# Optimization experiments

Hardware: AMD Instinct MI355X
Metric: run time of the kernel (lower is better)

## Reference

```python
import jax, jax.numpy as jnp
import numpy as np

D = 1024
H = 16
HD = D // H
B = 2
T = 2048


def setup_inputs() -> dict:
    key = jax.random.key(0)
    ks = jax.random.split(key, 5)
    x = jax.random.normal(ks[0], (B, T, D), dtype=jnp.float32)
    # PyTorch SDPA bool-mask semantics: True = attend. Causal lower-triangular.
    attn_mask = jnp.tril(jnp.ones((T, T), dtype=bool))
    w_qkv = jax.random.normal(ks[1], (3 * D, D), dtype=jnp.float32) * (1.0 / np.sqrt(D))
    b_qkv = jax.random.normal(ks[2], (3 * D,), dtype=jnp.float32) * 0.02
    w_proj = jax.random.normal(ks[3], (D, D), dtype=jnp.float32) * (1.0 / np.sqrt(D))
    b_proj = jax.random.normal(ks[4], (D,), dtype=jnp.float32) * 0.02
    return {"x": x, "attn_mask": attn_mask, "w_qkv": w_qkv, "b_qkv": b_qkv,
            "w_proj": w_proj, "b_proj": b_proj}


def reference(x, attn_mask, w_qkv, b_qkv, w_proj, b_proj):
    b, t, d = x.shape
    # fused QKV projection (torch Linear: y = x @ W.T + b)
    qkv = jnp.einsum('btd,ed->bte', x, w_qkv) + b_qkv  # [B,T,3D]
    q, k, v = jnp.split(qkv, 3, axis=-1)
    # [B,T,D] -> [B,H,T,hd]
    def heads(z):
        return z.reshape(b, t, H, HD).transpose(0, 2, 1, 3)
    q, k, v = heads(q), heads(k), heads(v)
    scale = 1.0 / jnp.sqrt(jnp.asarray(HD, dtype=x.dtype))
    scores = jnp.einsum('bhqd,bhkd->bhqk', q, k) * scale  # [B,H,T,T]
    neg_inf = jnp.asarray(jnp.finfo(x.dtype).min, dtype=x.dtype)
    scores = jnp.where(attn_mask, scores, neg_inf)
    attn = jax.nn.softmax(scores, axis=-1)
    y = jnp.einsum('bhqk,bhkd->bhqd', attn, v)  # [B,H,T,hd]
    y = y.transpose(0, 2, 1, 3).reshape(b, t, d)
    y = jnp.einsum('btd,ed->bte', y, w_proj) + b_proj
    return y
```

## Files before the change

kernel.cpp:

```cpp
#include <hip/hip_runtime.h>
#include <hip/hip_bf16.h>
#include <math.h>

#define D_MODEL 1024
#define NHEAD   16
#define HDIM    64
#define BATCH   2
#define SEQ     2048
#define MTOT    (BATCH * SEQ)

typedef unsigned short u16;
typedef unsigned int u32;
typedef short short8 __attribute__((ext_vector_type(8)));
typedef float floatx4 __attribute__((ext_vector_type(4)));

#define LOG2E 1.44269504088896340736f

#if __has_builtin(__builtin_amdgcn_exp2f)
#define EXP2(x) __builtin_amdgcn_exp2f(x)
#else
#define EXP2(x) exp2f(x)
#endif

static __device__ __forceinline__ u16 f2b(float f) {
  union { __hip_bfloat16 h; u16 u; } cv;
  cv.h = __float2bfloat16(f);
  return cv.u;
}

typedef const __attribute__((address_space(1))) unsigned int guint;
typedef __attribute__((address_space(3))) unsigned int luint;
static __device__ __forceinline__ void gl_lds16(const u16* g, u16* l) {
  __builtin_amdgcn_global_load_lds((guint*)g, (luint*)l, 16, 0, 0);
}

__global__ __launch_bounds__(256) void cast3_f2b(
    const float* __restrict__ a, u16* __restrict__ ao, int na,
    const float* __restrict__ b, u16* __restrict__ bo, int nb,
    const float* __restrict__ c, u16* __restrict__ co) {
  int i = (blockIdx.x * 256 + threadIdx.x) * 4;
  const float* src;
  u16* dst;
  if (i < na) {
    src = a + i;
    dst = ao + i;
  } else if (i < na + nb) {
    src = b + (i - na);
    dst = bo + (i - na);
  } else {
    src = c + (i - na - nb);
    dst = co + (i - na - nb);
  }
  float4 v = *(const float4*)src;
  ushort4 o;
  o.x = f2b(v.x);
  o.y = f2b(v.y);
  o.z = f2b(v.z);
  o.w = f2b(v.w);
  *(ushort4*)dst = o;
}

template <int MODE, int AR>
__global__ __launch_bounds__(256) void gemm_bt_bf16(
    const u16* __restrict__ A, const u16* __restrict__ Bm,
    const float* __restrict__ bias, u16* __restrict__ Cq, u16* __restrict__ Ck,
    u16* __restrict__ Cvt, float* __restrict__ Cf, int M, int N, int K) {
  constexpr int MI = AR / 32;
  constexpr int SMREQ = 2 * (AR + 128) * 32;
  constexpr int SM = (MODE == 0) ? (SMREQ > 17408 ? SMREQ : 17408) : SMREQ;
  __shared__ u16 smem[SM];
  u16(*As)[AR][32] = (u16(*)[AR][32])smem;
  u16(*Bs)[128][32] = (u16(*)[128][32])(smem + 2 * AR * 32);

  const int tid = threadIdx.x;
  const int lane = tid & 63;
  const int wave = tid >> 6;
  const int wm = (wave >> 1) * (AR / 2);
  const int wn = (wave & 1) * 64;
  const int quad = lane >> 4;
  const int l15 = lane & 15;
  const int m0 = blockIdx.y * AR;
  const int n0 = blockIdx.x * 128;

  const int srow = wave * 16 + (lane >> 2);
  const int k8 = (lane & 3) * 8;

  const u16* gA0 = A + (size_t)(m0 + srow) * K + k8;
  const u16* gA1 = A + (size_t)(m0 + srow + 64) * K + k8;
  const u16* gB0 = Bm + (size_t)(n0 + srow) * K + k8;
  const u16* gB1 = Bm + (size_t)(n0 + srow + 64) * K + k8;

  floatx4 acc[MI][4];
#pragma unroll
  for (int i = 0; i < MI; ++i)
#pragma unroll
    for (int j = 0; j < 4; ++j)
#pragma unroll
      for (int e = 0; e < 4; ++e) acc[i][j][e] = 0.0f;

  gl_lds16(gA0, &As[0][srow][k8]);
  if (AR == 128) gl_lds16(gA1, &As[0][srow + 64][k8]);
  gl_lds16(gB0, &Bs[0][srow][k8]);
  gl_lds16(gB1, &Bs[0][srow + 64][k8]);

  const int niter = K / 32;
  for (int kt = 0; kt < niter; ++kt) {
    const int cur = kt & 1;
    __syncthreads();
    if (kt + 1 < niter) {
      const int k0n = (kt + 1) * 32;
      gl_lds16(gA0 + k0n, &As[cur ^ 1][srow][k8]);
      if (AR == 128) gl_lds16(gA1 + k0n, &As[cur ^ 1][srow + 64][k8]);
      gl_lds16(gB0 + k0n, &Bs[cur ^ 1][srow][k8]);
      gl_lds16(gB1 + k0n, &Bs[cur ^ 1][srow + 64][k8]);
    }
    short8 af[MI], bf[4];
#pragma unroll
    for (int i = 0; i < MI; ++i)
      af[i] = *(const short8*)&As[cur][wm + i * 16 + l15][quad * 8];
#pragma unroll
    for (int j = 0; j < 4; ++j)
      bf[j] = *(const short8*)&Bs[cur][wn + j * 16 + l15][quad * 8];
#pragma unroll
    for (int i = 0; i < MI; ++i)
#pragma unroll
      for (int j = 0; j < 4; ++j)
        acc[i][j] = __builtin_amdgcn_mfma_f32_16x16x32_bf16(af[i], bf[j],
                                                            acc[i][j], 0, 0, 0);
  }

  if (MODE == 0) {
    const int nbase = n0 + wn;
    const int sel = nbase >> 10;
    const int h = (nbase >> 6) & (NHEAD - 1);
    if (sel == 2) {
#pragma unroll
      for (int j = 0; j < 4; ++j) {
        const int n = nbase + j * 16 + l15;
        const float bv = bias[n];
        const int d = n & (HDIM - 1);
#pragma unroll
        for (int i = 0; i < MI; ++i) {
          const int mb = m0 + wm + i * 16 + quad * 4;
          const int b = mb >> 11;
          const int t = mb & (SEQ - 1);
          ushort4 o4;
          o4.x = f2b(acc[i][j][0] + bv);
          o4.y = f2b(acc[i][j][1] + bv);
          o4.z = f2b(acc[i][j][2] + bv);
          o4.w = f2b(acc[i][j][3] + bv);
          *(ushort4*)(Cvt + ((size_t)(b * NHEAD + h) * HDIM + d) * SEQ + t) = o4;
        }
      }
    } else {
      u16* dst = (sel == 0) ? Cq : Ck;
      __syncthreads();
      u16(*Ct)[68] = (u16(*)[68])(smem + wave * 4352);
#pragma unroll
      for (int j = 0; j < 4; ++j) {
        const float bv = bias[nbase + j * 16 + l15];
#pragma unroll
        for (int i = 0; i < MI; ++i)
#pragma unroll
          for (int r = 0; r < 4; ++r)
            Ct[i * 16 + quad * 4 + r][j * 16 + l15] = f2b(acc[i][j][r] + bv);
      }
      const int mb0 = m0 + wm;
      const int b = mb0 >> 11;
      const int t0 = mb0 & (SEQ - 1);
      u16* rowbase = dst + ((size_t)(b * NHEAD + h) * SEQ + t0) * HDIM;
      const int tr = lane >> 3;
      const int d8 = (lane & 7) * 8;
#pragma unroll
      for (int p = 0; p < 8; ++p) {
        const int row = p * 8 + tr;
        *(short8*)(rowbase + (size_t)row * HDIM + d8) =
            *(const short8*)&Ct[row][d8];
      }
    }
  } else {
#pragma unroll
    for (int j = 0; j < 4; ++j) {
      const int n = n0 + wn + j * 16 + l15;
      const float bv = bias[n];
#pragma unroll
      for (int i = 0; i < MI; ++i) {
        const int mb = m0 + wm + i * 16 + quad * 4;
#pragma unroll
        for (int r = 0; r < 4; ++r)
          Cf[(size_t)(mb + r) * N + n] = acc[i][j][r] + bv;
      }
    }
  }
}

__global__ __launch_bounds__(256) void flash_mfma(const u16* __restrict__ Qg,
                                                  const u16* __restrict__ Kg,
                                                  const u16* __restrict__ Vtg,
                                                  u16* __restrict__ Yb) {
  __shared__ u16 Ks[2][64][76];
  __shared__ u16 Vt[2][80][76];
  __shared__ u16 Pb[64][76];

  const int tid = threadIdx.x;
  const int lane = tid & 63;
  const int wave = tid >> 6;
  const int wrow = wave * 16;
  const int quad = lane >> 4;
  const int l15 = lane & 15;
  const int bh = blockIdx.y;
  const int b = bh >> 4;
  const int h = bh & (NHEAD - 1);

  const u16* Qp = Qg + (size_t)bh * SEQ * HDIM;
  const u16* Kp = Kg + (size_t)bh * SEQ * HDIM;
  const u16* Vp = Vtg + (size_t)bh * HDIM * SEQ;

  const int srow = tid >> 2;
  const int sc = (tid & 3) * 16;

  const float scale2 = 0.125f * LOG2E;

#pragma unroll
  for (int bufi = 0; bufi < 2; ++bufi)
    for (int idx = tid; idx < 16 * 38; idx += 256) {
      const int row = 64 + idx / 38;
      const int c2 = (idx % 38) * 2;
      *(u32*)&Vt[bufi][row][c2] = (row == 64 && c2 < 64) ? 0x3F803F80u : 0u;
    }

#pragma unroll
  for (int phase = 0; phase < 2; ++phase) {
    const int qt = phase == 0 ? (16 + blockIdx.x) : (15 - blockIdx.x);
    const int q0 = qt * 64;

    __syncthreads();

    short8 aq[2];
    {
      const u16* qrow = Qp + (size_t)(q0 + wrow + l15) * HDIM + quad * 8;
      aq[0] = *(const short8*)qrow;
      aq[1] = *(const short8*)(qrow + 32);
    }

    floatx4 o[5];
#pragma unroll
    for (int c = 0; c < 5; ++c)
#pragma unroll
      for (int e = 0; e < 4; ++e) o[c][e] = 0.0f;

    const int nkt = qt + 1;
    short8 kv0 = *(const short8*)(Kp + (size_t)srow * HDIM + sc);
    short8 kv1 = *(const short8*)(Kp + (size_t)srow * HDIM + sc + 8);
    short8 vv0 = *(const short8*)(Vp + (size_t)srow * SEQ + sc);
    short8 vv1 = *(const short8*)(Vp + (size_t)srow * SEQ + sc + 8);

    for (int kt = 0; kt < nkt; ++kt) {
      const int k0 = kt * 64;
      const int buf = kt & 1;
      *(short8*)&Ks[buf][srow][sc] = kv0;
      *(short8*)&Ks[buf][srow][sc + 8] = kv1;
      *(short8*)&Vt[buf][srow][sc] = vv0;
      *(short8*)&Vt[buf][srow][sc + 8] = vv1;
      __syncthreads();
      if (kt + 1 < nkt) {
        const u16* kp = Kp + (size_t)(k0 + 64 + srow) * HDIM + sc;
        const u16* vp = Vp + (size_t)srow * SEQ + k0 + 64 + sc;
        kv0 = *(const short8*)kp;
        kv1 = *(const short8*)(kp + 8);
        vv0 = *(const short8*)vp;
        vv1 = *(const short8*)(vp + 8);
      }

      short8 bk[4][2];
#pragma unroll
      for (int c = 0; c < 4; ++c)
#pragma unroll
        for (int kk = 0; kk < 2; ++kk)
          bk[c][kk] =
              *(const short8*)&Ks[buf][c * 16 + l15][kk * 32 + quad * 8];

      floatx4 s[4];
#pragma unroll
      for (int c = 0; c < 4; ++c) {
#pragma unroll
        for (int e = 0; e < 4; ++e) s[c][e] = 0.0f;
        s[c] = __builtin_amdgcn_mfma_f32_16x16x32_bf16(aq[0], bk[c][0], s[c],
                                                       0, 0, 0);
        s[c] = __builtin_amdgcn_mfma_f32_16x16x32_bf16(aq[1], bk[c][1], s[c],
                                                       0, 0, 0);
      }

      const bool msk = (kt == nkt - 1);
      const int prow = wrow + quad * 4;
#pragma unroll
      for (int c = 0; c < 4; ++c)
#pragma unroll
        for (int r = 0; r < 4; ++r) {
          float v = s[c][r] * scale2;
          if (msk) {
            const int row = q0 + prow + r;
            const int col = k0 + c * 16 + l15;
            if (col > row) v = -INFINITY;
          }
          Pb[prow + r][c * 16 + l15] = f2b(EXP2(v));
        }

      short8 ap[2];
#pragma unroll
      for (int kk = 0; kk < 2; ++kk)
        ap[kk] = *(const short8*)&Pb[wrow + l15][kk * 32 + quad * 8];
#pragma unroll
      for (int c = 0; c < 5; ++c) {
        short8 bv0 = *(const short8*)&Vt[buf][c * 16 + l15][quad * 8];
        short8 bv1 = *(const short8*)&Vt[buf][c * 16 + l15][32 + quad * 8];
        o[c] = __builtin_amdgcn_mfma_f32_16x16x32_bf16(ap[0], bv0, o[c], 0, 0,
                                                       0);
        o[c] = __builtin_amdgcn_mfma_f32_16x16x32_bf16(ap[1], bv1, o[c], 0, 0,
                                                       0);
      }
    }

#pragma unroll
    for (int r = 0; r < 4; ++r) {
      const float lr = __shfl(o[4][r], lane & 48);
      const float inv = 1.0f / lr;
      const int t = q0 + wrow + quad * 4 + r;
#pragma unroll
      for (int c = 0; c < 4; ++c)
        Yb[((size_t)b * SEQ + t) * D_MODEL + h * HDIM + c * 16 + l15] =
            f2b(o[c][r] * inv);
    }
  }
}

extern "C" void kernel_launch(void* const* d_in, const int* in_sizes, int n_in,
                              void* d_out, int out_size, void* d_ws,
                              size_t ws_size, hipStream_t stream) {
  const float* x = (const float*)d_in[0];
  const float* w_qkv = (const float*)d_in[2];
  const float* b_qkv = (const float*)d_in[3];
  const float* w_proj = (const float*)d_in[4];
  const float* b_proj = (const float*)d_in[5];
  float* out = (float*)d_out;

  const size_t nx = (size_t)MTOT * D_MODEL;
  const size_t nwq = (size_t)3 * D_MODEL * D_MODEL;
  const size_t nwp = (size_t)D_MODEL * D_MODEL;
  const size_t nqkv = (size_t)BATCH * NHEAD * SEQ * HDIM;

  u16* xb = (u16*)d_ws;
  u16* wqb = xb + nx;
  u16* wpb = wqb + nwq;
  u16* qb = wpb + nwp;
  u16* kb = qb + nqkv;
  u16* vtb = kb + nqkv;
  u16* yb = vtb + nqkv;

  cast3_f2b<<<dim3((nx + nwq + nwp) / 1024), dim3(256), 0, stream>>>(
      x, xb, (int)nx, w_qkv, wqb, (int)nwq, w_proj, wpb);

  gemm_bt_bf16<0, 128><<<dim3(24, 32), dim3(256), 0, stream>>>(
      xb, wqb, b_qkv, qb, kb, vtb, nullptr, MTOT, 3 * D_MODEL, D_MODEL);
  flash_mfma<<<dim3(16, BATCH * NHEAD), dim3(256), 0, stream>>>(qb, kb, vtb,
                                                                yb);
  gemm_bt_bf16<1, 64><<<dim3(8, 64), dim3(256), 0, stream>>>(
      yb, wpb, b_proj, nullptr, nullptr, nullptr, out, MTOT, D_MODEL, D_MODEL);
}
```

Measured before the change: 188.7 us.

## Split flash attention KV tiles across wave pairs and keep P in registers

Restructures the flash attention kernel so that two wave pairs each process alternate 64-key tiles of a two-tile super-step. Each wave owns 32 query rows and computes S transposed so the P fragments can feed a 16x16x16 MFMA directly from registers, which removes the LDS round-trip for P. The row sum is now accumulated explicitly instead of through the extra ones-row V column, and the partial outputs of the two wave pairs are merged through an LDS scratch buffer at the end. This adds an extra barrier per step, wasted work on the odd final tile, and a reduction epilogue.

```diff
diff --git a/kernel.cpp b/kernel.cpp
--- a/kernel.cpp
+++ b/kernel.cpp
@@ -12,6 +12,7 @@
 typedef unsigned short u16;
 typedef unsigned int u32;
 typedef short short8 __attribute__((ext_vector_type(8)));
+typedef short short4v __attribute__((ext_vector_type(4)));
 typedef float floatx4 __attribute__((ext_vector_type(4)));
 
 #define LOG2E 1.44269504088896340736f
@@ -26,6 +27,18 @@
   union { __hip_bfloat16 h; u16 u; } cv;
   cv.h = __float2bfloat16(f);
   return cv.u;
+}
+
+static __device__ __forceinline__ floatx4 mfma16(short4v a, short4v b,
+                                                 floatx4 c) {
+#if __has_builtin(__builtin_amdgcn_mfma_f32_16x16x16bf16_1k)
+  return __builtin_amdgcn_mfma_f32_16x16x16bf16_1k(a, b, c, 0, 0, 0);
+#else
+  asm volatile("v_mfma_f32_16x16x16_bf16 %0, %1, %2, %0"
+               : "+v"(c)
+               : "v"(a), "v"(b));
+  return c;
+#endif
 }
 
 typedef const __attribute__((address_space(1))) unsigned int guint;
@@ -198,14 +211,15 @@
                                                   const u16* __restrict__ Kg,
                                                   const u16* __restrict__ Vtg,
                                                   u16* __restrict__ Yb) {
-  __shared__ u16 Ks[2][64][76];
-  __shared__ u16 Vt[2][80][76];
-  __shared__ u16 Pb[64][76];
+  __shared__ u16 Ks[2][64][72];
+  __shared__ u16 Vt[2][64][72];
+  __shared__ float scr[2][64][36];
 
   const int tid = threadIdx.x;
   const int lane = tid & 63;
   const int wave = tid >> 6;
-  const int wrow = wave * 16;
+  const int par = wave >> 1;
+  const int rhalf = (wave & 1) * 32;
   const int quad = lane >> 4;
   const int l15 = lane & 15;
   const int bh = blockIdx.y;
@@ -217,119 +231,175 @@
   const u16* Vp = Vtg + (size_t)bh * HDIM * SEQ;
 
   const int srow = tid >> 2;
-  const int sc = (tid & 3) * 16;
+  const int scq = (tid & 3) * 16;
 
   const float scale2 = 0.125f * LOG2E;
-
-#pragma unroll
-  for (int bufi = 0; bufi < 2; ++bufi)
-    for (int idx = tid; idx < 16 * 38; idx += 256) {
-      const int row = 64 + idx / 38;
-      const int c2 = (idx % 38) * 2;
-      *(u32*)&Vt[bufi][row][c2] = (row == 64 && c2 < 64) ? 0x3F803F80u : 0u;
-    }
 
 #pragma unroll
   for (int phase = 0; phase < 2; ++phase) {
     const int qt = phase == 0 ? (16 + blockIdx.x) : (15 - blockIdx.x);
     const int q0 = qt * 64;
-
+    const int nkt = qt + 1;
+    const int nsup = (nkt + 1) >> 1;
+
+    short8 aq[2][2];
+#pragma unroll
+    for (int m = 0; m < 2; ++m) {
+      const u16* qrow =
+          Qp + (size_t)(q0 + rhalf + m * 16 + l15) * HDIM + quad * 8;
+      aq[m][0] = *(const short8*)qrow;
+      aq[m][1] = *(const short8*)(qrow + 32);
+    }
+
+    floatx4 o[2][4];
+#pragma unroll
+    for (int m = 0; m < 2; ++m)
+#pragma unroll
+      for (int cd = 0; cd < 4; ++cd)
+#pragma unroll
+        for (int e = 0; e < 4; ++e) o[m][cd][e] = 0.0f;
+    float l_acc[2] = {0.0f, 0.0f};
+
+    short8 rk[2][2], rv[2][2];
+    {
+#pragma unroll
+      for (int t = 0; t < 2; ++t) {
+        const int kb = (t < nkt ? t : nkt - 1) * 64;
+        const u16* kp = Kp + (size_t)(kb + srow) * HDIM + scq;
+        const u16* vp = Vp + (size_t)srow * SEQ + kb + scq;
+        rk[t][0] = *(const short8*)kp;
+        rk[t][1] = *(const short8*)(kp + 8);
+        rv[t][0] = *(const short8*)vp;
+        rv[t][1] = *(const short8*)(vp + 8);
+      }
+    }
+
+    for (int s2 = 0; s2 < nsup; ++s2) {
+#pragma unroll
+      for (int t = 0; t < 2; ++t) {
+        *(short8*)&Ks[t][srow][scq] = rk[t][0];
+        *(short8*)&Ks[t][srow][scq + 8] = rk[t][1];
+        *(short8*)&Vt[t][srow][scq] = rv[t][0];
+        *(short8*)&Vt[t][srow][scq + 8] = rv[t][1];
+      }
+      __syncthreads();
+      if (s2 + 1 < nsup) {
+#pragma unroll
+        for (int t = 0; t < 2; ++t) {
+          const int kt = 2 * s2 + 2 + t;
+          const int kb = (kt < nkt ? kt : nkt - 1) * 64;
+          const u16* kp = Kp + (size_t)(kb + srow) * HDIM + scq;
+          const u16* vp = Vp + (size_t)srow * SEQ + kb + scq;
+          rk[t][0] = *(const short8*)kp;
+          rk[t][1] = *(const short8*)(kp + 8);
+          rv[t][0] = *(const short8*)vp;
+          rv[t][1] = *(const short8*)(vp + 8);
+        }
+      }
+
+      const int my_kt = 2 * s2 + par;
+      if (my_kt < nkt) {
+        const int k0p = my_kt * 64;
+
+        floatx4 st[4][2];
+#pragma unroll
+        for (int ck = 0; ck < 4; ++ck) {
+          const u16* krow = &Ks[par][ck * 16 + l15][quad * 8];
+          const short8 bk0 = *(const short8*)krow;
+          const short8 bk1 = *(const short8*)(krow + 32);
+#pragma unroll
+          for (int m = 0; m < 2; ++m) {
+            floatx4 acc;
+#pragma unroll
+            for (int e = 0; e < 4; ++e) acc[e] = 0.0f;
+            acc = __builtin_amdgcn_mfma_f32_16x16x32_bf16(bk0, aq[m][0], acc,
+                                                          0, 0, 0);
+            acc = __builtin_amdgcn_mfma_f32_16x16x32_bf16(bk1, aq[m][1], acc,
+                                                          0, 0, 0);
+            st[ck][m] = acc;
+          }
+        }
+
+        const bool msk = (my_kt == qt);
+        short4v pl[4][2];
+#pragma unroll
+        for (int ck = 0; ck < 4; ++ck)
+#pragma unroll
+          for (int m = 0; m < 2; ++m) {
+            const int qrow = q0 + rhalf + m * 16 + l15;
+            const int kbase = k0p + ck * 16 + quad * 4;
+            float psum = 0.0f;
+            short4v pv;
+#pragma unroll
+            for (int r = 0; r < 4; ++r) {
+              float p = EXP2(st[ck][m][r] * scale2);
+              if (msk && (kbase + r > qrow)) p = 0.0f;
+              psum += p;
+              pv[r] = (short)f2b(p);
+            }
+            l_acc[m] += psum;
+            pl[ck][m] = pv;
+          }
+
+#pragma unroll
+        for (int ck = 0; ck < 4; ++ck) {
+          short4v bv[4];
+#pragma unroll
+          for (int cd = 0; cd < 4; ++cd)
+            bv[cd] =
+                *(const short4v*)&Vt[par][cd * 16 + l15][ck * 16 + quad * 4];
+#pragma unroll
+          for (int m = 0; m < 2; ++m)
+#pragma unroll
+            for (int cd = 0; cd < 4; ++cd)
+              o[m][cd] = mfma16(pl[ck][m], bv[cd], o[m][cd]);
+        }
+      }
+      __syncthreads();
+    }
+
+#pragma unroll
+    for (int m = 0; m < 2; ++m) {
+      l_acc[m] += __shfl_xor(l_acc[m], 16);
+      l_acc[m] += __shfl_xor(l_acc[m], 32);
+    }
+
+    if (wave >= 2) {
+      float* sp = &scr[wave & 1][lane][0];
+#pragma unroll
+      for (int m = 0; m < 2; ++m)
+#pragma unroll
+        for (int cd = 0; cd < 4; ++cd)
+          *(floatx4*)(sp + (m * 4 + cd) * 4) = o[m][cd];
+      sp[32] = l_acc[0];
+      sp[33] = l_acc[1];
+    }
     __syncthreads();
-
-    short8 aq[2];
-    {
-      const u16* qrow = Qp + (size_t)(q0 + wrow + l15) * HDIM + quad * 8;
-      aq[0] = *(const short8*)qrow;
-      aq[1] = *(const short8*)(qrow + 32);
-    }
-
-    floatx4 o[5];
-#pragma unroll
-    for (int c = 0; c < 5; ++c)
-#pragma unroll
-      for (int e = 0; e < 4; ++e) o[c][e] = 0.0f;
-
-    const int nkt = qt + 1;
-    short8 kv0 = *(const short8*)(Kp + (size_t)srow * HDIM + sc);
-    short8 kv1 = *(const short8*)(Kp + (size_t)srow * HDIM + sc + 8);
-    short8 vv0 = *(const short8*)(Vp + (size_t)srow * SEQ + sc);
-    short8 vv1 = *(const short8*)(Vp + (size_t)srow * SEQ + sc + 8);
-
-    for (int kt = 0; kt < nkt; ++kt) {
-      const int k0 = kt * 64;
-      const int buf = kt & 1;
-      *(short8*)&Ks[buf][srow][sc] = kv0;
-      *(short8*)&Ks[buf][srow][sc + 8] = kv1;
-      *(short8*)&Vt[buf][srow][sc] = vv0;
-      *(short8*)&Vt[buf][srow][sc + 8] = vv1;
-      __syncthreads();
-      if (kt + 1 < nkt) {
-        const u16* kp = Kp + (size_t)(k0 + 64 + srow) * HDIM + sc;
-        const u16* vp = Vp + (size_t)srow * SEQ + k0 + 64 + sc;
-        kv0 = *(const short8*)kp;
-        kv1 = *(const short8*)(kp + 8);
-        vv0 = *(const short8*)vp;
-        vv1 = *(const short8*)(vp + 8);
-      }
-
-      short8 bk[4][2];
-#pragma unroll
-      for (int c = 0; c < 4; ++c)
-#pragma unroll
-        for (int kk = 0; kk < 2; ++kk)
-          bk[c][kk] =
-              *(const short8*)&Ks[buf][c * 16 + l15][kk * 32 + quad * 8];
-
-      floatx4 s[4];
-#pragma unroll
-      for (int c = 0; c < 4; ++c) {
-#pragma unroll
-        for (int e = 0; e < 4; ++e) s[c][e] = 0.0f;
-        s[c] = __builtin_amdgcn_mfma_f32_16x16x32_bf16(aq[0], bk[c][0], s[c],
-                                                       0, 0, 0);
-        s[c] = __builtin_amdgcn_mfma_f32_16x16x32_bf16(aq[1], bk[c][1], s[c],
-                                                       0, 0, 0);
-      }
-
-      const bool msk = (kt == nkt - 1);
-      const int prow = wrow + quad * 4;
-#pragma unroll
-      for (int c = 0; c < 4; ++c)
+    if (wave < 2) {
+      const float* sp = &scr[wave][lane][0];
+#pragma unroll
+      for (int m = 0; m < 2; ++m)
+#pragma unroll
+        for (int cd = 0; cd < 4; ++cd) {
+          const floatx4 t = *(const floatx4*)(sp + (m * 4 + cd) * 4);
+#pragma unroll
+          for (int e = 0; e < 4; ++e) o[m][cd][e] += t[e];
+        }
+      l_acc[0] += sp[32];
+      l_acc[1] += sp[33];
+
+#pragma unroll
+      for (int m = 0; m < 2; ++m)
 #pragma unroll
         for (int r = 0; r < 4; ++r) {
-          float v = s[c][r] * scale2;
-          if (msk) {
-            const int row = q0 + prow + r;
-            const int col = k0 + c * 16 + l15;
-            if (col > row) v = -INFINITY;
-          }
-          Pb[prow + r][c * 16 + l15] = f2b(EXP2(v));
-        }
-
-      short8 ap[2];
-#pragma unroll
-      for (int kk = 0; kk < 2; ++kk)
-        ap[kk] = *(const short8*)&Pb[wrow + l15][kk * 32 + quad * 8];
-#pragma unroll
-      for (int c = 0; c < 5; ++c) {
-        short8 bv0 = *(const short8*)&Vt[buf][c * 16 + l15][quad * 8];
-        short8 bv1 = *(const short8*)&Vt[buf][c * 16 + l15][32 + quad * 8];
-        o[c] = __builtin_amdgcn_mfma_f32_16x16x32_bf16(ap[0], bv0, o[c], 0, 0,
-                                                       0);
-        o[c] = __builtin_amdgcn_mfma_f32_16x16x32_bf16(ap[1], bv1, o[c], 0, 0,
-                                                       0);
-      }
-    }
-
-#pragma unroll
-    for (int r = 0; r < 4; ++r) {
-      const float lr = __shfl(o[4][r], lane & 48);
-      const float inv = 1.0f / lr;
-      const int t = q0 + wrow + quad * 4 + r;
-#pragma unroll
-      for (int c = 0; c < 4; ++c)
-        Yb[((size_t)b * SEQ + t) * D_MODEL + h * HDIM + c * 16 + l15] =
-            f2b(o[c][r] * inv);
+          const float lv = __shfl(l_acc[m], quad * 4 + r);
+          const float inv = 1.0f / lv;
+          const int t = q0 + rhalf + m * 16 + quad * 4 + r;
+#pragma unroll
+          for (int cd = 0; cd < 4; ++cd)
+            Yb[((size_t)b * SEQ + t) * D_MODEL + h * HDIM + cd * 16 + l15] =
+                f2b(o[m][cd][r] * inv);
+        }
     }
   }
 }
```

After: 189.2 us. Within noise of the previous version (+0.3%).

## Restructure flash attention to LDS-free per-wave 16-row tiles with register P

Applied to the files above, without the earlier changes.

Rewrites the attention kernel so each wave independently handles a 16-query-row strip, reading K and V straight from global memory instead of staging them in shared memory. It computes S transposed, so the exponentiated probabilities land in registers laid out as the A operand of a 16x16x16 MFMA, which removes the LDS round trip for P. Row sums are accumulated with shuffles instead of the ones-column trick, masking is done at 16-column granularity, and setprio hints wrap the MFMAs. The cost is no K/V reuse across waves within a block, so more global/L2 traffic and exposed load latency, plus a smaller 128-thread block and a finer causal grid.

```diff
diff --git a/kernel.cpp b/kernel.cpp
--- a/kernel.cpp
+++ b/kernel.cpp
@@ -12,6 +12,7 @@
 typedef unsigned short u16;
 typedef unsigned int u32;
 typedef short short8 __attribute__((ext_vector_type(8)));
+typedef short short4v __attribute__((ext_vector_type(4)));
 typedef float floatx4 __attribute__((ext_vector_type(4)));
 
 #define LOG2E 1.44269504088896340736f
@@ -26,6 +27,18 @@
   union { __hip_bfloat16 h; u16 u; } cv;
   cv.h = __float2bfloat16(f);
   return cv.u;
+}
+
+static __device__ __forceinline__ floatx4 mfma16(short4v a, short4v b,
+                                                 floatx4 c) {
+#if __has_builtin(__builtin_amdgcn_mfma_f32_16x16x16bf16_1k)
+  return __builtin_amdgcn_mfma_f32_16x16x16bf16_1k(a, b, c, 0, 0, 0);
+#else
+  asm volatile("v_mfma_f32_16x16x16_bf16 %0, %1, %2, %0"
+               : "+v"(c)
+               : "v"(a), "v"(b));
+  return c;
+#endif
 }
 
 typedef const __attribute__((address_space(1))) unsigned int guint;
@@ -194,21 +207,70 @@
   }
 }
 
-__global__ __launch_bounds__(256) void flash_mfma(const u16* __restrict__ Qg,
+template <bool MSK>
+static __device__ __forceinline__ void attn_tile(
+    const u16* __restrict__ Kp, const u16* __restrict__ Vp, int k0, int ckmax,
+    int qrow, short8 aq0, short8 aq1, int quad, int l15, floatx4* o,
+    float& l_acc) {
+  const float scale2 = 0.125f * LOG2E;
+  short4v pl[4];
+  floatx4 st[4];
+#pragma unroll
+  for (int ck = 0; ck < 4; ++ck) {
+    if (MSK && ck >= ckmax) continue;
+    const u16* krow = Kp + (size_t)(k0 + ck * 16 + l15) * HDIM + quad * 8;
+    const short8 bk0 = *(const short8*)krow;
+    const short8 bk1 = *(const short8*)(krow + 32);
+    floatx4 acc;
+#pragma unroll
+    for (int e = 0; e < 4; ++e) acc[e] = 0.0f;
+    __builtin_amdgcn_s_setprio(1);
+    acc = __builtin_amdgcn_mfma_f32_16x16x32_bf16(bk0, aq0, acc, 0, 0, 0);
+    acc = __builtin_amdgcn_mfma_f32_16x16x32_bf16(bk1, aq1, acc, 0, 0, 0);
+    __builtin_amdgcn_s_setprio(0);
+    st[ck] = acc;
+  }
+#pragma unroll
+  for (int ck = 0; ck < 4; ++ck) {
+    if (MSK && ck >= ckmax) continue;
+    const int kbase = k0 + ck * 16 + quad * 4;
+    float psum = 0.0f;
+    short4v pv;
+#pragma unroll
+    for (int r = 0; r < 4; ++r) {
+      float p = EXP2(st[ck][r] * scale2);
+      if (MSK && (kbase + r > qrow)) p = 0.0f;
+      psum += p;
+      pv[r] = (short)f2b(p);
+    }
+    l_acc += psum;
+    pl[ck] = pv;
+  }
+#pragma unroll
+  for (int ck = 0; ck < 4; ++ck) {
+    if (MSK && ck >= ckmax) continue;
+    short4v bv[4];
+#pragma unroll
+    for (int cd = 0; cd < 4; ++cd)
+      bv[cd] = *(const short4v*)(Vp + (size_t)(cd * 16 + l15) * SEQ + k0 +
+                                 ck * 16 + quad * 4);
+    __builtin_amdgcn_s_setprio(1);
+#pragma unroll
+    for (int cd = 0; cd < 4; ++cd) o[cd] = mfma16(pl[ck], bv[cd], o[cd]);
+    __builtin_amdgcn_s_setprio(0);
+  }
+}
+
+__global__ __launch_bounds__(128) void flash_mfma(const u16* __restrict__ Qg,
                                                   const u16* __restrict__ Kg,
                                                   const u16* __restrict__ Vtg,
                                                   u16* __restrict__ Yb) {
-  __shared__ u16 Ks[2][64][76];
-  __shared__ u16 Vt[2][80][76];
-  __shared__ u16 Pb[64][76];
-
-  const int tid = threadIdx.x;
-  const int lane = tid & 63;
-  const int wave = tid >> 6;
-  const int wrow = wave * 16;
+  const int lane = threadIdx.x & 63;
+  const int wave = threadIdx.x >> 6;
   const int quad = lane >> 4;
   const int l15 = lane & 15;
-  const int bh = blockIdx.y;
+  const int bh = blockIdx.x >> 5;
+  const int j = ((blockIdx.x & 31) << 1) | wave;
   const int b = bh >> 4;
   const int h = bh & (NHEAD - 1);
 
@@ -216,120 +278,42 @@
   const u16* Kp = Kg + (size_t)bh * SEQ * HDIM;
   const u16* Vp = Vtg + (size_t)bh * HDIM * SEQ;
 
-  const int srow = tid >> 2;
-  const int sc = (tid & 3) * 16;
-
-  const float scale2 = 0.125f * LOG2E;
-
-#pragma unroll
-  for (int bufi = 0; bufi < 2; ++bufi)
-    for (int idx = tid; idx < 16 * 38; idx += 256) {
-      const int row = 64 + idx / 38;
-      const int c2 = (idx % 38) * 2;
-      *(u32*)&Vt[bufi][row][c2] = (row == 64 && c2 < 64) ? 0x3F803F80u : 0u;
-    }
-
 #pragma unroll
   for (int phase = 0; phase < 2; ++phase) {
-    const int qt = phase == 0 ? (16 + blockIdx.x) : (15 - blockIdx.x);
-    const int q0 = qt * 64;
-
-    __syncthreads();
-
-    short8 aq[2];
-    {
-      const u16* qrow = Qp + (size_t)(q0 + wrow + l15) * HDIM + quad * 8;
-      aq[0] = *(const short8*)qrow;
-      aq[1] = *(const short8*)(qrow + 32);
-    }
-
-    floatx4 o[5];
-#pragma unroll
-    for (int c = 0; c < 5; ++c)
-#pragma unroll
-      for (int e = 0; e < 4; ++e) o[c][e] = 0.0f;
-
-    const int nkt = qt + 1;
-    short8 kv0 = *(const short8*)(Kp + (size_t)srow * HDIM + sc);
-    short8 kv1 = *(const short8*)(Kp + (size_t)srow * HDIM + sc + 8);
-    short8 vv0 = *(const short8*)(Vp + (size_t)srow * SEQ + sc);
-    short8 vv1 = *(const short8*)(Vp + (size_t)srow * SEQ + sc + 8);
-
-    for (int kt = 0; kt < nkt; ++kt) {
-      const int k0 = kt * 64;
-      const int buf = kt & 1;
-      *(short8*)&Ks[buf][srow][sc] = kv0;
-      *(short8*)&Ks[buf][srow][sc + 8] = kv1;
-      *(short8*)&Vt[buf][srow][sc] = vv0;
-      *(short8*)&Vt[buf][srow][sc + 8] = vv1;
-      __syncthreads();
-      if (kt + 1 < nkt) {
-        const u16* kp = Kp + (size_t)(k0 + 64 + srow) * HDIM + sc;
-        const u16* vp = Vp + (size_t)srow * SEQ + k0 + 64 + sc;
-        kv0 = *(const short8*)kp;
-        kv1 = *(const short8*)(kp + 8);
-        vv0 = *(const short8*)vp;
-        vv1 = *(const short8*)(vp + 8);
-      }
-
-      short8 bk[4][2];
-#pragma unroll
-      for (int c = 0; c < 4; ++c)
-#pragma unroll
-        for (int kk = 0; kk < 2; ++kk)
-          bk[c][kk] =
-              *(const short8*)&Ks[buf][c * 16 + l15][kk * 32 + quad * 8];
-
-      floatx4 s[4];
-#pragma unroll
-      for (int c = 0; c < 4; ++c) {
-#pragma unroll
-        for (int e = 0; e < 4; ++e) s[c][e] = 0.0f;
-        s[c] = __builtin_amdgcn_mfma_f32_16x16x32_bf16(aq[0], bk[c][0], s[c],
-                                                       0, 0, 0);
-        s[c] = __builtin_amdgcn_mfma_f32_16x16x32_bf16(aq[1], bk[c][1], s[c],
-                                                       0, 0, 0);
-      }
-
-      const bool msk = (kt == nkt - 1);
-      const int prow = wrow + quad * 4;
-#pragma unroll
-      for (int c = 0; c < 4; ++c)
-#pragma unroll
-        for (int r = 0; r < 4; ++r) {
-          float v = s[c][r] * scale2;
-          if (msk) {
-            const int row = q0 + prow + r;
-            const int col = k0 + c * 16 + l15;
-            if (col > row) v = -INFINITY;
-          }
-          Pb[prow + r][c * 16 + l15] = f2b(EXP2(v));
-        }
-
-      short8 ap[2];
-#pragma unroll
-      for (int kk = 0; kk < 2; ++kk)
-        ap[kk] = *(const short8*)&Pb[wrow + l15][kk * 32 + quad * 8];
-#pragma unroll
-      for (int c = 0; c < 5; ++c) {
-        short8 bv0 = *(const short8*)&Vt[buf][c * 16 + l15][quad * 8];
-        short8 bv1 = *(const short8*)&Vt[buf][c * 16 + l15][32 + quad * 8];
-        o[c] = __builtin_amdgcn_mfma_f32_16x16x32_bf16(ap[0], bv0, o[c], 0, 0,
-                                                       0);
-        o[c] = __builtin_amdgcn_mfma_f32_16x16x32_bf16(ap[1], bv1, o[c], 0, 0,
-                                                       0);
-      }
-    }
+    const int s = phase == 0 ? (64 + j) : (63 - j);
+    const int q0 = s * 16;
+    const int nkt = (s >> 2) + 1;
+    const int qrow = q0 + l15;
+
+    const u16* qp = Qp + (size_t)qrow * HDIM + quad * 8;
+    const short8 aq0 = *(const short8*)qp;
+    const short8 aq1 = *(const short8*)(qp + 32);
+
+    floatx4 o[4];
+#pragma unroll
+    for (int cd = 0; cd < 4; ++cd)
+#pragma unroll
+      for (int e = 0; e < 4; ++e) o[cd][e] = 0.0f;
+    float l_acc = 0.0f;
+
+    for (int kt = 0; kt < nkt - 1; ++kt)
+      attn_tile<false>(Kp, Vp, kt * 64, 4, qrow, aq0, aq1, quad, l15, o,
+                       l_acc);
+    attn_tile<true>(Kp, Vp, (nkt - 1) * 64, (s & 3) + 1, qrow, aq0, aq1, quad,
+                    l15, o, l_acc);
+
+    l_acc += __shfl_xor(l_acc, 16);
+    l_acc += __shfl_xor(l_acc, 32);
 
 #pragma unroll
     for (int r = 0; r < 4; ++r) {
-      const float lr = __shfl(o[4][r], lane & 48);
-      const float inv = 1.0f / lr;
-      const int t = q0 + wrow + quad * 4 + r;
-#pragma unroll
-      for (int c = 0; c < 4; ++c)
-        Yb[((size_t)b * SEQ + t) * D_MODEL + h * HDIM + c * 16 + l15] =
-            f2b(o[c][r] * inv);
+      const float lv = __shfl(l_acc, quad * 4 + r);
+      const float inv = 1.0f / lv;
+      const int t = q0 + quad * 4 + r;
+#pragma unroll
+      for (int cd = 0; cd < 4; ++cd)
+        Yb[((size_t)b * SEQ + t) * D_MODEL + h * HDIM + cd * 16 + l15] =
+            f2b(o[cd][r] * inv);
     }
   }
 }
@@ -362,8 +346,7 @@
 
   gemm_bt_bf16<0, 128><<<dim3(24, 32), dim3(256), 0, stream>>>(
       xb, wqb, b_qkv, qb, kb, vtb, nullptr, MTOT, 3 * D_MODEL, D_MODEL);
-  flash_mfma<<<dim3(16, BATCH * NHEAD), dim3(256), 0, stream>>>(qb, kb, vtb,
-                                                                yb);
+  flash_mfma<<<dim3(1024), dim3(128), 0, stream>>>(qb, kb, vtb, yb);
   gemm_bt_bf16<1, 64><<<dim3(8, 64), dim3(256), 0, stream>>>(
       yb, wpb, b_proj, nullptr, nullptr, nullptr, out, MTOT, D_MODEL, D_MODEL);
 }
```

New measurement: 317.2 us. +68.1%, slower.
